# Kernel tuning notes

Measured on AMD Instinct MI355X. Metric: run time of the kernel, lower is better.

## Reference

```python
import jax, jax.numpy as jnp
import numpy as np

NTYPES = 2
MAXNEI = 100
MNT = MAXNEI * NTYPES  # max_neighbor * ntypes = 200
RMIN = 0.5
RMAX = 6.0
M1 = 100   # last embedding width
M2 = 16
FH = 240   # fitting hidden width
NPHYS = 4
TFEAT = 8
B, NAT = 4, 1024


def mlp_resnet(x, Ws, bs):
    # DeepMD-style MLP: tanh layers with identity / duplicated-identity resnet
    for W, b in zip(Ws, bs):
        h = jnp.tanh(x @ W + b)
        if h.shape[-1] == x.shape[-1]:
            h = h + x
        elif h.shape[-1] == 2 * x.shape[-1]:
            h = h + jnp.concatenate([x, x], axis=-1)
        x = h
    return x


def setup_inputs() -> dict:
    key = jax.random.key(0)
    ks = jax.random.split(key, 24)
    r = jax.random.uniform(ks[0], (B, NAT, MNT), minval=0.1, maxval=7.0)
    pad = jax.random.uniform(ks[1], (B, NAT, MNT)) < 0.25
    r = jnp.where(pad, 0.0, r)
    d = jax.random.normal(ks[2], (B, NAT, MNT, 3))
    d = d / jnp.linalg.norm(d, axis=-1, keepdims=True)
    ImageDR = jnp.concatenate([r[..., None], r[..., None] * d], axis=-1).astype(jnp.float32)

    list_neigh = jax.random.randint(ks[3], (B, NAT, MNT), 0, MAXNEI)
    Imagetype_map = jax.random.randint(ks[4], (NAT,), 0, NTYPES).astype(jnp.int32)
    type_map = jnp.array([3, 14], dtype=jnp.int64)

    davg = (0.1 * jax.random.normal(ks[5], (NTYPES, MNT, 4))).astype(jnp.float32)
    dstd = (1.0 + 0.1 * jax.random.uniform(ks[6], (NTYPES, MNT, 4))).astype(jnp.float32)

    def w(k, shape):
        return (jax.random.normal(k, shape) / np.sqrt(shape[-2] if len(shape) > 1 else 1.0)).astype(jnp.float32)

    type_vector = jax.random.normal(ks[7], (NTYPES, NPHYS)).astype(jnp.float32)
    tW0 = w(ks[8], (NPHYS, TFEAT)); tb0 = jnp.zeros((TFEAT,), jnp.float32)
    eW0 = w(ks[9], (1 + TFEAT, 25)); eb0 = jnp.zeros((25,), jnp.float32)
    eW1 = w(ks[10], (25, 50));       eb1 = jnp.zeros((50,), jnp.float32)
    eW2 = w(ks[11], (50, M1));       eb2 = jnp.zeros((M1,), jnp.float32)
    fW0 = w(ks[12], (NTYPES, M2 * M1, FH)); fb0 = jnp.zeros((NTYPES, FH), jnp.float32)
    fW1 = w(ks[13], (NTYPES, FH, FH));      fb1 = jnp.zeros((NTYPES, FH), jnp.float32)
    fW2 = w(ks[14], (NTYPES, FH, FH));      fb2 = jnp.zeros((NTYPES, FH), jnp.float32)
    fWf = w(ks[15], (NTYPES, FH, 1))
    energy_shift = jnp.array([-3.2, -5.1], jnp.float32).reshape(NTYPES, 1)
    fbf = (0.01 * jax.random.normal(ks[16], (NTYPES, 1))).astype(jnp.float32) + energy_shift

    return dict(list_neigh=list_neigh, Imagetype_map=Imagetype_map, type_map=type_map,
                ImageDR=ImageDR, nghost=0, davg=davg, dstd=dstd, type_vector=type_vector,
                tW0=tW0, tb0=tb0, eW0=eW0, eb0=eb0, eW1=eW1, eb1=eb1, eW2=eW2, eb2=eb2,
                fW0=fW0, fb0=fb0, fW1=fW1, fb1=fb1, fW2=fW2, fb2=fb2, fWf=fWf, fbf=fbf)


def _forward(ImageDR, davg, dstd, type_vector, tW0, tb0, eW0, eb0, eW1, eb1, eW2, eb2,
             fW0, fb0, fW1, fb1, fW2, fb2, fWf, fbf, Imagetype_map):
    r = ImageDR[..., 0]
    r_safe = jnp.where(r > 1e-5, r, 1.0)
    inv_r = 1.0 / r_safe
    u = (r - RMIN) / (RMAX - RMIN)
    s_mid = inv_r * (u ** 3 * (-6.0 * u ** 2 + 15.0 * u - 10.0) + 1.0)
    Srij = jnp.where((r > 0) & (r < RMIN), inv_r,
                     jnp.where((r >= RMIN) & (r < RMAX), s_mid, 0.0))  # (B,N,J)
    mask = (jnp.abs(r) > 1e-5)[..., None]
    Ri = jnp.concatenate([Srij[..., None],
                          jnp.where(mask, Srij[..., None] * ImageDR[..., 1:4] * inv_r[..., None], 0.0)],
                         axis=-1)  # (B,N,J,4)
    # per-atom-type normalization
    Ri = (Ri - davg[Imagetype_map][None]) / dstd[Imagetype_map][None]

    # neighbor type feature from type-embedding net
    nt_idx = jnp.arange(MNT) // MAXNEI              # (J,) neighbor slot -> type
    tfeat = mlp_resnet(type_vector, [tW0], [tb0])   # (ntypes, TFEAT)
    nf = jnp.broadcast_to(tfeat[nt_idx][None, None], Ri.shape[:3] + (TFEAT,))
    x = jnp.concatenate([Ri[..., 0:1], nf], axis=-1)            # (B,N,J,1+TFEAT)
    G = mlp_resnet(x, [eW0, eW1, eW2], [eb0, eb1, eb2])         # (B,N,J,M1)

    xyz = jnp.einsum('bnjd,bnjm->bndm', Ri, G) / MNT            # (B,N,4,M1)
    DR = jnp.einsum('bndm,bndq->bnmq', xyz, xyz[..., :M2])      # (B,N,M1,M2)
    DR = DR.reshape(DR.shape[0], DR.shape[1], M1 * M2)

    Ei = jnp.zeros(DR.shape[:2], DR.dtype)
    for t in range(NTYPES):  # per-type fitting nets
        h = mlp_resnet(DR, [fW0[t], fW1[t], fW2[t]], [fb0[t], fb1[t], fb2[t]])
        e = (h @ fWf[t] + fbf[t])[..., 0]
        Ei = jnp.where(Imagetype_map[None, :] == t, e, Ei)
    Etot = jnp.sum(Ei, axis=1, keepdims=True)  # (B,1)
    return Etot, Ei


def reference(list_neigh, Imagetype_map, type_map, ImageDR, nghost, davg, dstd, type_vector,
              tW0, tb0, eW0, eb0, eW1, eb1, eW2, eb2,
              fW0, fb0, fW1, fb1, fW2, fb2, fWf, fbf):
    # list_neigh/type_map/nghost only participate in force computation (is_calc_f=False path)
    return _forward(ImageDR, davg, dstd, type_vector, tW0, tb0, eW0, eb0, eW1, eb1, eW2, eb2,
                    fW0, fb0, fW1, fb1, fW2, fb2, fWf, fbf, Imagetype_map)
```

## Files before the change

kernel.cpp:

```cpp
#include <hip/hip_runtime.h>
#include <hip/hip_bf16.h>

#define NATC  1024
#define BATCH 4
#define MNTC  200
#define M1C   100
#define M2C   16
#define FHC   240
#define KPAD  256
#define HSTR  264
#define H1STR 40
#define H2STR 72
#define NR    128

typedef __attribute__((ext_vector_type(8))) short bf16x8;
typedef __attribute__((ext_vector_type(4))) float f32x4;

__device__ __forceinline__ float fast_tanh(float x){
    float e = __expf(2.0f * x);
    float r = __fdividef(1.0f, e + 1.0f);
    return fmaf(-2.0f, r, 1.0f);
}

__device__ __forceinline__ unsigned short f2bf(float x){
    __hip_bfloat16 h = __float2bfloat16(x);
    return *reinterpret_cast<unsigned short*>(&h);
}

__device__ __forceinline__ float bf2f(unsigned short u){
    unsigned int v = ((unsigned int)u) << 16;
    return *reinterpret_cast<float*>(&v);
}

__device__ __forceinline__ unsigned int pack2(float a, float b){
    return (unsigned int)f2bf(a) | ((unsigned int)f2bf(b) << 16);
}

__global__ __launch_bounds__(256) void part_kernel(const int* __restrict__ tmap,
                                                   int* __restrict__ idx,
                                                   int* __restrict__ counts){
    __shared__ int s0[256], s1[256];
    const int tid = threadIdx.x;
    int ty[4]; int c0 = 0, c1 = 0;
    #pragma unroll
    for (int r = 0; r < 4; ++r){
        ty[r] = tmap[tid*4 + r];
        if (ty[r] == 0) c0++; else c1++;
    }
    s0[tid] = c0; s1[tid] = c1;
    __syncthreads();
    for (int off = 1; off < 256; off <<= 1){
        int v0 = (tid >= off) ? s0[tid-off] : 0;
        int v1 = (tid >= off) ? s1[tid-off] : 0;
        __syncthreads();
        s0[tid] += v0; s1[tid] += v1;
        __syncthreads();
    }
    int e0 = s0[tid] - c0, e1 = s1[tid] - c1;
    #pragma unroll
    for (int r = 0; r < 4; ++r){
        int n = tid*4 + r;
        if (ty[r] == 0) idx[e0++] = n; else idx[NATC + e1++] = n;
    }
    if (tid == 255){ counts[0] = s0[255]; counts[1] = s1[255]; }
}

__global__ __launch_bounds__(256) void transp_kernel(const float* __restrict__ src,
                                                     unsigned short* __restrict__ dst,
                                                     int K, int N, int Kpad, int nkt, int nnt){
    __shared__ float tile[64][65];
    const int tid = threadIdx.x;
    int bid = blockIdx.x;
    const int t  = bid / (nkt*nnt);
    bid -= t*nkt*nnt;
    const int kt = bid / nnt;
    const int nt = bid - kt*nnt;
    const float* s = src + (size_t)t*K*N;
    unsigned short* d = dst + (size_t)t*N*Kpad;

    const int c  = tid & 63;
    const int rg = tid >> 6;
    #pragma unroll
    for (int p = 0; p < 16; ++p){
        int row = p*4 + rg;
        int gr = kt*64 + row, gc = nt*64 + c;
        tile[row][c] = (gr < K && gc < N) ? s[(size_t)gr*N + gc] : 0.0f;
    }
    __syncthreads();
    const int nn0 = tid >> 3;
    const int k8  = (tid & 7) * 8;
    #pragma unroll
    for (int p = 0; p < 2; ++p){
        int nn = p*32 + nn0;
        int gn = nt*64 + nn;
        int gk = kt*64 + k8;
        if (gn < N && gk < Kpad){
            unsigned short v[8];
            #pragma unroll
            for (int j = 0; j < 8; ++j) v[j] = f2bf(tile[k8+j][nn]);
            *(bf16x8*)(d + (size_t)gn*Kpad + gk) = *(bf16x8*)v;
        }
    }
}

__global__ __launch_bounds__(256) void prep_kernel(const float* __restrict__ tv,
                                                   const float* __restrict__ tW0,
                                                   const float* __restrict__ tb0,
                                                   const float* __restrict__ eW0,
                                                   const float* __restrict__ eb0,
                                                   const float* __restrict__ eW1,
                                                   const float* __restrict__ eW2,
                                                   unsigned short* __restrict__ ew1t,
                                                   unsigned short* __restrict__ ew2t,
                                                   float* __restrict__ Tb){
    __shared__ float tfl[16];
    const int tid = threadIdx.x;
    if (tid < 16){
        int t = tid >> 3, f = tid & 7;
        float s = tb0[f];
        #pragma unroll
        for (int p = 0; p < 4; ++p) s = fmaf(tv[t*4+p], tW0[p*8+f], s);
        tfl[tid] = fast_tanh(s) + tv[t*4 + (f & 3)];
    }
    __syncthreads();
    if (tid < 64){
        int t = tid >> 5, o = tid & 31;
        if (o < 25){
            float s = eb0[o];
            #pragma unroll
            for (int k = 0; k < 8; ++k) s = fmaf(tfl[t*8 + k], eW0[(k+1)*25 + o], s);
            Tb[t*32 + o] = s;
        } else {
            Tb[t*32 + o] = 0.0f;
        }
    }
    for (int i = tid; i < 112*64; i += 256){
        int n = i >> 6, k = i & 63;
        ew2t[i] = (n < M1C && k < 50) ? f2bf(eW2[(size_t)k*M1C + n]) : (unsigned short)0;
    }
    for (int i = tid; i < 64*32; i += 256){
        int n = i >> 5, k = i & 31;
        ew1t[i] = (n < 50 && k < 25) ? f2bf(eW1[(size_t)k*50 + n]) : (unsigned short)0;
    }
}

__global__ __launch_bounds__(256, 4) void embed_kernel(
    const float4* __restrict__ imdr,
    const float4* __restrict__ davg,
    const float4* __restrict__ dstd,
    const int*    __restrict__ tmap,
    const float*  __restrict__ eW0,
    const float*  __restrict__ Tb,
    const float*  __restrict__ eb1,
    const float*  __restrict__ eb2,
    const unsigned short* __restrict__ ew1t,
    const unsigned short* __restrict__ ew2t,
    float* __restrict__ xyzg)
{
    __shared__ __align__(16) float Rif[NR][4];
    __shared__ __align__(16) unsigned short H1s[NR][H1STR];
    __shared__ __align__(16) unsigned short H2s[NR][H2STR];

    const int tid = threadIdx.x;
    const int bid = blockIdx.x;
    const int a   = bid >> 1;
    const int jh  = bid & 1;
    const int n0  = a & (NATC - 1);
    const int itype = tmap[n0];

    if (tid < NR){
        const int jg = jh*NR + tid;
        unsigned int* rowp = (unsigned int*)&H1s[tid][0];
        if (jg < MNTC){
            float4 dr = imdr[(size_t)a*MNTC + jg];
            float r  = dr.x;
            float rs = (r > 1e-5f) ? r : 1.0f;
            float ir = __fdividef(1.0f, rs);
            float u  = (r - 0.5f) * (1.0f/5.5f);
            float u2 = u*u, u3 = u2*u;
            float smid = ir * (u3 * (-6.0f*u2 + 15.0f*u - 10.0f) + 1.0f);
            float S = 0.0f;
            if (r > 0.0f && r < 0.5f)       S = ir;
            else if (r >= 0.5f && r < 6.0f) S = smid;
            bool msk = fabsf(r) > 1e-5f;
            float R0 = S;
            float R1 = msk ? S * dr.y * ir : 0.0f;
            float R2 = msk ? S * dr.z * ir : 0.0f;
            float R3 = msk ? S * dr.w * ir : 0.0f;
            float4 av = davg[itype*MNTC + jg];
            float4 sv = dstd[itype*MNTC + jg];
            float rin0 = __fdividef(R0 - av.x, sv.x);
            float rin1 = __fdividef(R1 - av.y, sv.y);
            float rin2 = __fdividef(R2 - av.z, sv.z);
            float rin3 = __fdividef(R3 - av.w, sv.w);
            Rif[tid][0] = rin0; Rif[tid][1] = rin1; Rif[tid][2] = rin2; Rif[tid][3] = rin3;

            const float* tb = Tb + ((jg >= 100) ? 32 : 0);
            float h1[25];
            #pragma unroll
            for (int o = 0; o < 25; ++o)
                h1[o] = fast_tanh(fmaf(rin0, eW0[o], tb[o]));

            #pragma unroll
            for (int c = 0; c < 12; ++c) rowp[c] = pack2(h1[2*c], h1[2*c+1]);
            rowp[12] = (unsigned int)f2bf(h1[24]);
            #pragma unroll
            for (int c = 13; c < 20; ++c) rowp[c] = 0u;
        } else {
            Rif[tid][0] = 0.0f; Rif[tid][1] = 0.0f; Rif[tid][2] = 0.0f; Rif[tid][3] = 0.0f;
            #pragma unroll
            for (int c = 0; c < 20; ++c) rowp[c] = 0u;
        }
    }
    __syncthreads();

    const int lane = tid & 63;
    const int w    = tid >> 6;
    const int lc   = lane & 15;
    const int lg   = lane >> 4;

    #pragma unroll
    for (int mi = 0; mi < 2; ++mi){
        const int mt = w + mi*4;
        bf16x8 af = *(const bf16x8*)&H1s[mt*16 + lc][lg*8];
        const int rbase = mt*16 + lg*4;
        #pragma unroll
        for (int nt = 0; nt < 4; ++nt){
            const int n = nt*16 + lc;
            const bool live = (n < 50);
            float bv = live ? eb1[n] : 0.0f;
            f32x4 c;
            c[0] = bv; c[1] = bv; c[2] = bv; c[3] = bv;
            bf16x8 bfr = *(const bf16x8*)(ew1t + n*32 + lg*8);
            c = __builtin_amdgcn_mfma_f32_16x16x32_bf16(af, bfr, c, 0, 0, 0);
            const int rc = n % 25;
            #pragma unroll
            for (int i = 0; i < 4; ++i){
                const int row = rbase + i;
                unsigned short v = 0;
                if (live) v = f2bf(fast_tanh(c[i]) + bf2f(H1s[row][rc]));
                H2s[row][n] = v;
            }
        }
    }
    __syncthreads();

    float* xyzp = (float*)&H1s[0][0];

    #pragma unroll
    for (int half = 0; half < 2; ++half){
        const int ntbase = half * 4;
        float xacc[4][4];
        #pragma unroll
        for (int q = 0; q < 4; ++q)
            #pragma unroll
            for (int d = 0; d < 4; ++d) xacc[q][d] = 0.0f;

        #pragma unroll
        for (int mi = 0; mi < 2; ++mi){
            const int mt = w + mi*4;
            const int rbase = mt*16 + lg*4;
            float4 rj[4];
            #pragma unroll
            for (int i = 0; i < 4; ++i) rj[i] = *(const float4*)&Rif[rbase + i][0];
            const unsigned short* arow = &H2s[mt*16 + lc][0];
            bf16x8 a0 = *(const bf16x8*)(arow + lg*8);
            bf16x8 a1 = *(const bf16x8*)(arow + 32 + lg*8);
            #pragma unroll
            for (int q = 0; q < 4; ++q){
                const int nt = ntbase + q;
                if (nt >= 7) continue;
                const int cg = nt*16 + lc;
                const unsigned short* bp = ew2t + (size_t)cg*64 + lg*8;
                bf16x8 b0 = *(const bf16x8*)(bp);
                bf16x8 b1 = *(const bf16x8*)(bp + 32);
                float bv = (cg < M1C) ? eb2[cg] : 0.0f;
                f32x4 c;
                c[0] = bv; c[1] = bv; c[2] = bv; c[3] = bv;
                c = __builtin_amdgcn_mfma_f32_16x16x32_bf16(a0, b0, c, 0, 0, 0);
                c = __builtin_amdgcn_mfma_f32_16x16x32_bf16(a1, b1, c, 0, 0, 0);
                const int rc = (cg >= 100) ? cg - 100 : ((cg >= 50) ? cg - 50 : cg);
                #pragma unroll
                for (int i = 0; i < 4; ++i){
                    float g = fast_tanh(c[i]) + bf2f(H2s[rbase + i][rc]);
                    xacc[q][0] = fmaf(g, rj[i].x, xacc[q][0]);
                    xacc[q][1] = fmaf(g, rj[i].y, xacc[q][1]);
                    xacc[q][2] = fmaf(g, rj[i].z, xacc[q][2]);
                    xacc[q][3] = fmaf(g, rj[i].w, xacc[q][3]);
                }
            }
        }
        #pragma unroll
        for (int q = 0; q < 4; ++q){
            const int nt = ntbase + q;
            if (nt >= 7) continue;
            #pragma unroll
            for (int d = 0; d < 4; ++d){
                float v = xacc[q][d];
                v += __shfl_xor(v, 16);
                v += __shfl_xor(v, 32);
                if (lane < 16) xyzp[((w*4 + d)*112) + nt*16 + lc] = v;
            }
        }
    }
    __syncthreads();

    for (int i = tid; i < 448; i += 256){
        int d = i / 112, m = i - d*112;
        xyzg[(size_t)a*896 + jh*448 + i] =
            xyzp[(0*4+d)*112 + m] + xyzp[(1*4+d)*112 + m] +
            xyzp[(2*4+d)*112 + m] + xyzp[(3*4+d)*112 + m];
    }
}

__global__ __launch_bounds__(256) void dr_kernel(const float* __restrict__ xyzg,
                                                 unsigned short* __restrict__ DRout){
    __shared__ float xyzs[448];
    const int a = blockIdx.x;
    const int tid = threadIdx.x;
    for (int i = tid; i < 448; i += 256)
        xyzs[i] = (xyzg[(size_t)a*896 + i] + xyzg[(size_t)a*896 + 448 + i]) * (1.0f / (float)MNTC);
    __syncthreads();
    if (tid < 200){
        const int i8 = tid * 8;
        const int m  = i8 >> 4;
        const int qb = i8 & 15;
        float xm[4], s[8];
        #pragma unroll
        for (int d = 0; d < 4; ++d) xm[d] = xyzs[d*112 + m];
        #pragma unroll
        for (int e = 0; e < 8; ++e){
            float acc = 0.0f;
            #pragma unroll
            for (int d = 0; d < 4; ++d) acc = fmaf(xm[d], xyzs[d*112 + qb + e], acc);
            s[e] = acc;
        }
        unsigned short v[8];
        #pragma unroll
        for (int e = 0; e < 8; ++e) v[e] = f2bf(s[e]);
        *(bf16x8*)(DRout + (size_t)a*(M1C*M2C) + i8) = *(bf16x8*)v;
    }
}

__global__ __launch_bounds__(512, 2) void fitm_kernel(
    const unsigned short* __restrict__ DRbf,
    const int*   __restrict__ idx,
    const int*   __restrict__ counts,
    const unsigned short* __restrict__ w0t,
    const unsigned short* __restrict__ w1t,
    const unsigned short* __restrict__ w2t,
    const float* __restrict__ fb0,
    const float* __restrict__ fb1,
    const float* __restrict__ fb2,
    const float* __restrict__ fWf,
    const float* __restrict__ fbf,
    float* __restrict__ out)
{
    const int bid = blockIdx.x;
    const int t = bid & 1;
    const int g = (bid >> 1) & 31;
    const int b = bid >> 6;
    const int cnt  = counts[t];
    const int base = g * 32;
    if (base >= cnt) return;
    const int na = min(32, cnt - base);

    __shared__ int ns[32];
    __shared__ __align__(16) unsigned short hA[32][HSTR];
    __shared__ __align__(16) unsigned short hB[32][HSTR];
    __shared__ float epart[8][32];

    const int tid  = threadIdx.x;
    const int lane = tid & 63;
    const int w    = tid >> 6;
    if (tid < 32) ns[tid] = idx[t*NATC + base + ((tid < na) ? tid : 0)];
    __syncthreads();

    const int lc = lane & 15;
    const int lg = lane >> 4;

    int   ncol[2];  bool act[2];
    #pragma unroll
    for (int nt = 0; nt < 2; ++nt){
        ncol[nt] = w*32 + nt*16 + lc;
        act[nt]  = (w*32 + nt*16) < FHC;
    }

    const unsigned short* aptr[2];
    aptr[0] = DRbf + ((size_t)(b*NATC + ns[lc]))*1600 + lg*8;
    aptr[1] = DRbf + ((size_t)(b*NATC + ns[16 + lc]))*1600 + lg*8;
    const unsigned short* bptr0[2];
    #pragma unroll
    for (int nt = 0; nt < 2; ++nt)
        bptr0[nt] = act[nt] ? (w0t + ((size_t)(t*FHC + ncol[nt]))*1600 + lg*8) : w0t;

    f32x4 acc[2][2];
    #pragma unroll
    for (int mi = 0; mi < 2; ++mi)
        #pragma unroll
        for (int nt = 0; nt < 2; ++nt){
            float bv = act[nt] ? fb0[t*FHC + ncol[nt]] : 0.0f;
            acc[mi][nt][0] = bv; acc[mi][nt][1] = bv; acc[mi][nt][2] = bv; acc[mi][nt][3] = bv;
        }
    #pragma unroll 4
    for (int ks = 0; ks < 50; ++ks){
        bf16x8 a0 = *(const bf16x8*)(aptr[0] + ks*32);
        bf16x8 a1 = *(const bf16x8*)(aptr[1] + ks*32);
        #pragma unroll
        for (int nt = 0; nt < 2; ++nt){
            if (act[nt]){
                bf16x8 bfg = *(const bf16x8*)(bptr0[nt] + ks*32);
                acc[0][nt] = __builtin_amdgcn_mfma_f32_16x16x32_bf16(a0, bfg, acc[0][nt], 0, 0, 0);
                acc[1][nt] = __builtin_amdgcn_mfma_f32_16x16x32_bf16(a1, bfg, acc[1][nt], 0, 0, 0);
            }
        }
    }
    float h0r[2][2][4];
    #pragma unroll
    for (int mi = 0; mi < 2; ++mi)
        #pragma unroll
        for (int nt = 0; nt < 2; ++nt)
            #pragma unroll
            for (int i = 0; i < 4; ++i){
                int row = mi*16 + lg*4 + i;
                if (act[nt]){
                    h0r[mi][nt][i] = fast_tanh(acc[mi][nt][i]);
                    hA[row][ncol[nt]] = f2bf(h0r[mi][nt][i]);
                } else {
                    h0r[mi][nt][i] = 0.0f;
                    hA[row][ncol[nt]] = 0;
                }
            }
    __syncthreads();

    f32x4 acc1[2][2];
    #pragma unroll
    for (int mi = 0; mi < 2; ++mi)
        #pragma unroll
        for (int nt = 0; nt < 2; ++nt){
            float bv = act[nt] ? fb1[t*FHC + ncol[nt]] : 0.0f;
            acc1[mi][nt][0] = bv; acc1[mi][nt][1] = bv; acc1[mi][nt][2] = bv; acc1[mi][nt][3] = bv;
        }
    const unsigned short* b1p[2];
    #pragma unroll
    for (int nt = 0; nt < 2; ++nt)
        b1p[nt] = act[nt] ? (w1t + ((size_t)(t*FHC + ncol[nt]))*KPAD + lg*8) : w1t;
    #pragma unroll
    for (int ks = 0; ks < 8; ++ks){
        bf16x8 a0 = *(const bf16x8*)&hA[lc][ks*32 + lg*8];
        bf16x8 a1 = *(const bf16x8*)&hA[16 + lc][ks*32 + lg*8];
        #pragma unroll
        for (int nt = 0; nt < 2; ++nt){
            if (act[nt]){
                bf16x8 bfg = *(const bf16x8*)(b1p[nt] + ks*32);
                acc1[0][nt] = __builtin_amdgcn_mfma_f32_16x16x32_bf16(a0, bfg, acc1[0][nt], 0, 0, 0);
                acc1[1][nt] = __builtin_amdgcn_mfma_f32_16x16x32_bf16(a1, bfg, acc1[1][nt], 0, 0, 0);
            }
        }
    }
    float h1r[2][2][4];
    #pragma unroll
    for (int mi = 0; mi < 2; ++mi)
        #pragma unroll
        for (int nt = 0; nt < 2; ++nt)
            #pragma unroll
            for (int i = 0; i < 4; ++i){
                int row = mi*16 + lg*4 + i;
                if (act[nt]){
                    h1r[mi][nt][i] = fast_tanh(acc1[mi][nt][i]) + h0r[mi][nt][i];
                    hB[row][ncol[nt]] = f2bf(h1r[mi][nt][i]);
                } else {
                    h1r[mi][nt][i] = 0.0f;
                    hB[row][ncol[nt]] = 0;
                }
            }
    __syncthreads();

    f32x4 acc2[2][2];
    #pragma unroll
    for (int mi = 0; mi < 2; ++mi)
        #pragma unroll
        for (int nt = 0; nt < 2; ++nt){
            float bv = act[nt] ? fb2[t*FHC + ncol[nt]] : 0.0f;
            acc2[mi][nt][0] = bv; acc2[mi][nt][1] = bv; acc2[mi][nt][2] = bv; acc2[mi][nt][3] = bv;
        }
    const unsigned short* b2p[2];
    #pragma unroll
    for (int nt = 0; nt < 2; ++nt)
        b2p[nt] = act[nt] ? (w2t + ((size_t)(t*FHC + ncol[nt]))*KPAD + lg*8) : w2t;
    #pragma unroll
    for (int ks = 0; ks < 8; ++ks){
        bf16x8 a0 = *(const bf16x8*)&hB[lc][ks*32 + lg*8];
        bf16x8 a1 = *(const bf16x8*)&hB[16 + lc][ks*32 + lg*8];
        #pragma unroll
        for (int nt = 0; nt < 2; ++nt){
            if (act[nt]){
                bf16x8 bfg = *(const bf16x8*)(b2p[nt] + ks*32);
                acc2[0][nt] = __builtin_amdgcn_mfma_f32_16x16x32_bf16(a0, bfg, acc2[0][nt], 0, 0, 0);
                acc2[1][nt] = __builtin_amdgcn_mfma_f32_16x16x32_bf16(a1, bfg, acc2[1][nt], 0, 0, 0);
            }
        }
    }

    float p[2][4];
    #pragma unroll
    for (int mi = 0; mi < 2; ++mi)
        #pragma unroll
        for (int i = 0; i < 4; ++i) p[mi][i] = 0.0f;
    #pragma unroll
    for (int nt = 0; nt < 2; ++nt){
        if (act[nt]){
            float wfv = fWf[t*FHC + ncol[nt]];
            #pragma unroll
            for (int mi = 0; mi < 2; ++mi)
                #pragma unroll
                for (int i = 0; i < 4; ++i){
                    float h = fast_tanh(acc2[mi][nt][i]) + h1r[mi][nt][i];
                    p[mi][i] = fmaf(h, wfv, p[mi][i]);
                }
        }
    }
    #pragma unroll
    for (int off = 1; off < 16; off <<= 1){
        #pragma unroll
        for (int mi = 0; mi < 2; ++mi)
            #pragma unroll
            for (int i = 0; i < 4; ++i)
                p[mi][i] += __shfl_xor(p[mi][i], off);
    }
    if (lc == 0){
        #pragma unroll
        for (int mi = 0; mi < 2; ++mi)
            #pragma unroll
            for (int i = 0; i < 4; ++i)
                epart[w][mi*16 + lg*4 + i] = p[mi][i];
    }
    __syncthreads();
    if (tid < 32){
        float e = fbf[t];
        #pragma unroll
        for (int ww = 0; ww < 8; ++ww) e += epart[ww][tid];
        float ee = 0.0f;
        if (tid < na){
            out[4 + b*NATC + ns[tid]] = e;
            ee = e;
        }
        #pragma unroll
        for (int off = 16; off >= 1; off >>= 1) ee += __shfl_down(ee, off, 32);
        if (tid == 0) atomicAdd(&out[b], ee);
    }
}

extern "C" void kernel_launch(void* const* d_in, const int* in_sizes, int n_in,
                              void* d_out, int out_size, void* d_ws, size_t ws_size,
                              hipStream_t stream)
{
    (void)in_sizes; (void)n_in; (void)out_size; (void)ws_size;
    const int*   tmap = (const int*)d_in[1];
    const float* imdr = (const float*)d_in[3];
    const float* davg = (const float*)d_in[5];
    const float* dstd = (const float*)d_in[6];
    const float* tv   = (const float*)d_in[7];
    const float* tW0  = (const float*)d_in[8];
    const float* tb0  = (const float*)d_in[9];
    const float* eW0  = (const float*)d_in[10];
    const float* eb0  = (const float*)d_in[11];
    const float* eW1  = (const float*)d_in[12];
    const float* eb1  = (const float*)d_in[13];
    const float* eW2  = (const float*)d_in[14];
    const float* eb2  = (const float*)d_in[15];
    const float* fW0  = (const float*)d_in[16];
    const float* fb0  = (const float*)d_in[17];
    const float* fW1  = (const float*)d_in[18];
    const float* fb1  = (const float*)d_in[19];
    const float* fW2  = (const float*)d_in[20];
    const float* fb2  = (const float*)d_in[21];
    const float* fWf  = (const float*)d_in[22];
    const float* fbf  = (const float*)d_in[23];
    float* out = (float*)d_out;

    char* ws = (char*)d_ws;
    int*   counts = (int*)ws;
    int*   idx    = (int*)(ws + 64);
    unsigned short* DRbf = (unsigned short*)(ws + 16384);
    unsigned short* w0t  = DRbf + (size_t)BATCH*NATC*1600;
    unsigned short* w1t  = w0t + (size_t)2*FHC*1600;
    unsigned short* w2t  = w1t + (size_t)2*FHC*KPAD;
    unsigned short* ew2t = w2t + (size_t)2*FHC*KPAD;
    unsigned short* ew1t = ew2t + 112*64;
    float* Tb            = (float*)(ew1t + 64*32);
    float* xyzg          = (float*)((char*)Tb + 4096);

    hipMemsetAsync(d_out, 0, 4*sizeof(float), stream);
    part_kernel<<<1, 256, 0, stream>>>(tmap, idx, counts);
    prep_kernel<<<1, 256, 0, stream>>>(tv, tW0, tb0, eW0, eb0, eW1, eW2, ew1t, ew2t, Tb);
    transp_kernel<<<2*25*4, 256, 0, stream>>>(fW0, w0t, 1600, FHC, 1600, 25, 4);
    transp_kernel<<<2*4*4,  256, 0, stream>>>(fW1, w1t, FHC, FHC, KPAD, 4, 4);
    transp_kernel<<<2*4*4,  256, 0, stream>>>(fW2, w2t, FHC, FHC, KPAD, 4, 4);
    embed_kernel<<<2*BATCH*NATC, 256, 0, stream>>>(
        (const float4*)imdr, (const float4*)davg, (const float4*)dstd, tmap,
        eW0, Tb, eb1, eb2, ew1t, ew2t, xyzg);
    dr_kernel<<<BATCH*NATC, 256, 0, stream>>>(xyzg, DRbf);
    fitm_kernel<<<256, 512, 0, stream>>>(
        DRbf, idx, counts, w0t, w1t, w2t, fb0, fb1, fb2, fWf, fbf, out);
}
```

Baseline: 373.2 us.

## Split fused fitting net into per-layer LDS-tiled GEMM kernels

Replaces the single fused three-layer fitting kernel with separate kernels. One handles layer 0 and another, launched twice, handles layers 1 and 2; each uses 64x64 LDS-staged tiles shared by four waves. Intermediate activations go through global bf16 buffers, and the final dot product is accumulated with atomics into a per-atom buffer that a small finish kernel scatters and sums. Weights are padded to 256 output rows so tiles need no bounds checks. The aim is better operand reuse and more parallel blocks, at the cost of extra launches, global round-trips for activations, and atomics.

```diff
diff --git a/kernel.cpp b/kernel.cpp
--- a/kernel.cpp
+++ b/kernel.cpp
@@ -7,11 +7,11 @@
 #define M1C   100
 #define M2C   16
 #define FHC   240
-#define KPAD  256
-#define HSTR  264
+#define NPAD  256
 #define H1STR 40
 #define H2STR 72
 #define NR    128
+#define ASTR  72
 
 typedef __attribute__((ext_vector_type(8))) short bf16x8;
 typedef __attribute__((ext_vector_type(4))) float f32x4;
@@ -67,7 +67,8 @@
 
 __global__ __launch_bounds__(256) void transp_kernel(const float* __restrict__ src,
                                                      unsigned short* __restrict__ dst,
-                                                     int K, int N, int Kpad, int nkt, int nnt){
+                                                     int K, int N, int Npad, int Kpad,
+                                                     int nkt, int nnt){
     __shared__ float tile[64][65];
     const int tid = threadIdx.x;
     int bid = blockIdx.x;
@@ -76,7 +77,7 @@
     const int kt = bid / nnt;
     const int nt = bid - kt*nnt;
     const float* s = src + (size_t)t*K*N;
-    unsigned short* d = dst + (size_t)t*N*Kpad;
+    unsigned short* d = dst + (size_t)t*Npad*Kpad;
 
     const int c  = tid & 63;
     const int rg = tid >> 6;
@@ -94,7 +95,7 @@
         int nn = p*32 + nn0;
         int gn = nt*64 + nn;
         int gk = kt*64 + k8;
-        if (gn < N && gk < Kpad){
+        if (gn < Npad && gk < Kpad){
             unsigned short v[8];
             #pragma unroll
             for (int j = 0; j < 8; ++j) v[j] = f2bf(tile[k8+j][nn]);
@@ -342,213 +343,204 @@
     }
 }
 
-__global__ __launch_bounds__(512, 2) void fitm_kernel(
+__global__ __launch_bounds__(256, 4) void fit_l0(
     const unsigned short* __restrict__ DRbf,
     const int*   __restrict__ idx,
     const int*   __restrict__ counts,
-    const unsigned short* __restrict__ w0t,
-    const unsigned short* __restrict__ w1t,
-    const unsigned short* __restrict__ w2t,
+    const unsigned short* __restrict__ w0p,
     const float* __restrict__ fb0,
-    const float* __restrict__ fb1,
-    const float* __restrict__ fb2,
-    const float* __restrict__ fWf,
-    const float* __restrict__ fbf,
-    float* __restrict__ out)
+    unsigned short* __restrict__ h0)
 {
-    const int bid = blockIdx.x;
+    int bid = blockIdx.x;
+    const int ntile = bid & 3; bid >>= 2;
+    const int mt = bid & 15;  bid >>= 4;
     const int t = bid & 1;
-    const int g = (bid >> 1) & 31;
-    const int b = bid >> 6;
-    const int cnt  = counts[t];
-    const int base = g * 32;
-    if (base >= cnt) return;
-    const int na = min(32, cnt - base);
-
-    __shared__ int ns[32];
-    __shared__ __align__(16) unsigned short hA[32][HSTR];
-    __shared__ __align__(16) unsigned short hB[32][HSTR];
-    __shared__ float epart[8][32];
-
-    const int tid  = threadIdx.x;
-    const int lane = tid & 63;
-    const int w    = tid >> 6;
-    if (tid < 32) ns[tid] = idx[t*NATC + base + ((tid < na) ? tid : 0)];
-    __syncthreads();
-
-    const int lc = lane & 15;
-    const int lg = lane >> 4;
-
-    int   ncol[2];  bool act[2];
-    #pragma unroll
-    for (int nt = 0; nt < 2; ++nt){
-        ncol[nt] = w*32 + nt*16 + lc;
-        act[nt]  = (w*32 + nt*16) < FHC;
-    }
-
-    const unsigned short* aptr[2];
-    aptr[0] = DRbf + ((size_t)(b*NATC + ns[lc]))*1600 + lg*8;
-    aptr[1] = DRbf + ((size_t)(b*NATC + ns[16 + lc]))*1600 + lg*8;
-    const unsigned short* bptr0[2];
-    #pragma unroll
-    for (int nt = 0; nt < 2; ++nt)
-        bptr0[nt] = act[nt] ? (w0t + ((size_t)(t*FHC + ncol[nt]))*1600 + lg*8) : w0t;
+    const int b = bid >> 1;
+    const int cnt = counts[t];
+    const int mbase = mt*64;
+    if (mbase >= cnt) return;
+
+    __shared__ int ns[64];
+    __shared__ __align__(16) unsigned short As[64][ASTR];
+    __shared__ __align__(16) unsigned short Bs[64][ASTR];
+
+    const int tid = threadIdx.x;
+    if (tid < 64) ns[tid] = idx[t*NATC + min(mbase + tid, cnt - 1)];
+    __syncthreads();
+
+    const int lane = tid & 63, w = tid >> 6;
+    const int wm = w >> 1, wn = w & 1;
+    const int lc = lane & 15, lg = lane >> 4;
+
+    const int srow = tid >> 3;
+    const int scol = (tid & 7) * 8;
+
+    const unsigned short* arow0 = DRbf + ((size_t)(b*NATC + ns[srow]))*1600;
+    const unsigned short* arow1 = DRbf + ((size_t)(b*NATC + ns[srow + 32]))*1600;
+    const unsigned short* brow0 = w0p + ((size_t)(t*NPAD + ntile*64 + srow))*1600;
+    const unsigned short* brow1 = w0p + ((size_t)(t*NPAD + ntile*64 + srow + 32))*1600;
 
     f32x4 acc[2][2];
     #pragma unroll
     for (int mi = 0; mi < 2; ++mi)
         #pragma unroll
-        for (int nt = 0; nt < 2; ++nt){
-            float bv = act[nt] ? fb0[t*FHC + ncol[nt]] : 0.0f;
-            acc[mi][nt][0] = bv; acc[mi][nt][1] = bv; acc[mi][nt][2] = bv; acc[mi][nt][3] = bv;
-        }
-    #pragma unroll 4
-    for (int ks = 0; ks < 50; ++ks){
-        bf16x8 a0 = *(const bf16x8*)(aptr[0] + ks*32);
-        bf16x8 a1 = *(const bf16x8*)(aptr[1] + ks*32);
-        #pragma unroll
-        for (int nt = 0; nt < 2; ++nt){
-            if (act[nt]){
-                bf16x8 bfg = *(const bf16x8*)(bptr0[nt] + ks*32);
-                acc[0][nt] = __builtin_amdgcn_mfma_f32_16x16x32_bf16(a0, bfg, acc[0][nt], 0, 0, 0);
-                acc[1][nt] = __builtin_amdgcn_mfma_f32_16x16x32_bf16(a1, bfg, acc[1][nt], 0, 0, 0);
+        for (int ni = 0; ni < 2; ++ni){
+            int col = ntile*64 + wn*32 + ni*16 + lc;
+            float bv = (col < FHC) ? fb0[t*FHC + col] : 0.0f;
+            acc[mi][ni][0] = bv; acc[mi][ni][1] = bv;
+            acc[mi][ni][2] = bv; acc[mi][ni][3] = bv;
+        }
+
+    for (int kc = 0; kc < 1600; kc += 64){
+        __syncthreads();
+        *(bf16x8*)&As[srow][scol]      = *(const bf16x8*)(arow0 + kc + scol);
+        *(bf16x8*)&As[srow + 32][scol] = *(const bf16x8*)(arow1 + kc + scol);
+        *(bf16x8*)&Bs[srow][scol]      = *(const bf16x8*)(brow0 + kc + scol);
+        *(bf16x8*)&Bs[srow + 32][scol] = *(const bf16x8*)(brow1 + kc + scol);
+        __syncthreads();
+        #pragma unroll
+        for (int kk = 0; kk < 2; ++kk){
+            bf16x8 a0 = *(const bf16x8*)&As[wm*32 + lc][kk*32 + lg*8];
+            bf16x8 a1 = *(const bf16x8*)&As[wm*32 + 16 + lc][kk*32 + lg*8];
+            bf16x8 b0 = *(const bf16x8*)&Bs[wn*32 + lc][kk*32 + lg*8];
+            bf16x8 b1 = *(const bf16x8*)&Bs[wn*32 + 16 + lc][kk*32 + lg*8];
+            acc[0][0] = __builtin_amdgcn_mfma_f32_16x16x32_bf16(a0, b0, acc[0][0], 0, 0, 0);
+            acc[0][1] = __builtin_amdgcn_mfma_f32_16x16x32_bf16(a0, b1, acc[0][1], 0, 0, 0);
+            acc[1][0] = __builtin_amdgcn_mfma_f32_16x16x32_bf16(a1, b0, acc[1][0], 0, 0, 0);
+            acc[1][1] = __builtin_amdgcn_mfma_f32_16x16x32_bf16(a1, b1, acc[1][1], 0, 0, 0);
+        }
+    }
+
+    const size_t Rseg = (size_t)((b*2 + t)*1024 + mbase);
+    #pragma unroll
+    for (int mi = 0; mi < 2; ++mi)
+        #pragma unroll
+        for (int ni = 0; ni < 2; ++ni){
+            int col = ntile*64 + wn*32 + ni*16 + lc;
+            #pragma unroll
+            for (int i = 0; i < 4; ++i){
+                int rowl = wm*32 + mi*16 + lg*4 + i;
+                h0[(Rseg + rowl)*NPAD + col] = f2bf(fast_tanh(acc[mi][ni][i]));
             }
         }
-    }
-    float h0r[2][2][4];
+}
+
+__global__ __launch_bounds__(256, 4) void fit_l12(
+    const unsigned short* __restrict__ h_in,
+    const int*   __restrict__ counts,
+    const unsigned short* __restrict__ wp,
+    const float* __restrict__ fb,
+    const float* __restrict__ wf,
+    unsigned short* __restrict__ h_out,
+    float* __restrict__ Ei_buf)
+{
+    int bid = blockIdx.x;
+    const int ntile = bid & 3; bid >>= 2;
+    const int mt = bid & 15;  bid >>= 4;
+    const int t = bid & 1;
+    const int b = bid >> 1;
+    const int cnt = counts[t];
+    const int mbase = mt*64;
+    if (mbase >= cnt) return;
+
+    __shared__ __align__(16) unsigned short As[64][ASTR];
+    __shared__ __align__(16) unsigned short Bs[64][ASTR];
+
+    const int tid = threadIdx.x;
+    const int lane = tid & 63, w = tid >> 6;
+    const int wm = w >> 1, wn = w & 1;
+    const int lc = lane & 15, lg = lane >> 4;
+
+    const int srow = tid >> 3;
+    const int scol = (tid & 7) * 8;
+
+    const size_t Rseg = (size_t)((b*2 + t)*1024 + mbase);
+    const unsigned short* arow0 = h_in + (Rseg + srow)*NPAD;
+    const unsigned short* arow1 = h_in + (Rseg + srow + 32)*NPAD;
+    const unsigned short* brow0 = wp + ((size_t)(t*NPAD + ntile*64 + srow))*NPAD;
+    const unsigned short* brow1 = wp + ((size_t)(t*NPAD + ntile*64 + srow + 32))*NPAD;
+
+    f32x4 acc[2][2];
     #pragma unroll
     for (int mi = 0; mi < 2; ++mi)
         #pragma unroll
-        for (int nt = 0; nt < 2; ++nt)
+        for (int ni = 0; ni < 2; ++ni){
+            int col = ntile*64 + wn*32 + ni*16 + lc;
+            float bv = (col < FHC) ? fb[t*FHC + col] : 0.0f;
+            acc[mi][ni][0] = bv; acc[mi][ni][1] = bv;
+            acc[mi][ni][2] = bv; acc[mi][ni][3] = bv;
+        }
+
+    for (int kc = 0; kc < 256; kc += 64){
+        __syncthreads();
+        *(bf16x8*)&As[srow][scol]      = *(const bf16x8*)(arow0 + kc + scol);
+        *(bf16x8*)&As[srow + 32][scol] = *(const bf16x8*)(arow1 + kc + scol);
+        *(bf16x8*)&Bs[srow][scol]      = *(const bf16x8*)(brow0 + kc + scol);
+        *(bf16x8*)&Bs[srow + 32][scol] = *(const bf16x8*)(brow1 + kc + scol);
+        __syncthreads();
+        #pragma unroll
+        for (int kk = 0; kk < 2; ++kk){
+            bf16x8 a0 = *(const bf16x8*)&As[wm*32 + lc][kk*32 + lg*8];
+            bf16x8 a1 = *(const bf16x8*)&As[wm*32 + 16 + lc][kk*32 + lg*8];
+            bf16x8 b0 = *(const bf16x8*)&Bs[wn*32 + lc][kk*32 + lg*8];
+            bf16x8 b1 = *(const bf16x8*)&Bs[wn*32 + 16 + lc][kk*32 + lg*8];
+            acc[0][0] = __builtin_amdgcn_mfma_f32_16x16x32_bf16(a0, b0, acc[0][0], 0, 0, 0);
+            acc[0][1] = __builtin_amdgcn_mfma_f32_16x16x32_bf16(a0, b1, acc[0][1], 0, 0, 0);
+            acc[1][0] = __builtin_amdgcn_mfma_f32_16x16x32_bf16(a1, b0, acc[1][0], 0, 0, 0);
+            acc[1][1] = __builtin_amdgcn_mfma_f32_16x16x32_bf16(a1, b1, acc[1][1], 0, 0, 0);
+        }
+    }
+
+    const bool fuse = (wf != nullptr);
+    #pragma unroll
+    for (int mi = 0; mi < 2; ++mi){
+        float pr[4] = {0.0f, 0.0f, 0.0f, 0.0f};
+        #pragma unroll
+        for (int ni = 0; ni < 2; ++ni){
+            int col = ntile*64 + wn*32 + ni*16 + lc;
+            float wfv = 0.0f;
+            if (fuse) wfv = (col < FHC) ? wf[t*FHC + col] : 0.0f;
             #pragma unroll
             for (int i = 0; i < 4; ++i){
-                int row = mi*16 + lg*4 + i;
-                if (act[nt]){
-                    h0r[mi][nt][i] = fast_tanh(acc[mi][nt][i]);
-                    hA[row][ncol[nt]] = f2bf(h0r[mi][nt][i]);
-                } else {
-                    h0r[mi][nt][i] = 0.0f;
-                    hA[row][ncol[nt]] = 0;
+                int rowl = wm*32 + mi*16 + lg*4 + i;
+                size_t gaddr = (Rseg + rowl)*NPAD + col;
+                float hv = fast_tanh(acc[mi][ni][i]) + bf2f(h_in[gaddr]);
+                if (!fuse) h_out[gaddr] = f2bf(hv);
+                else       pr[i] = fmaf(hv, wfv, pr[i]);
+            }
+        }
+        if (fuse){
+            #pragma unroll
+            for (int i = 0; i < 4; ++i){
+                float v = pr[i];
+                v += __shfl_xor(v, 1); v += __shfl_xor(v, 2);
+                v += __shfl_xor(v, 4); v += __shfl_xor(v, 8);
+                if (lc == 0){
+                    int rowl = wm*32 + mi*16 + lg*4 + i;
+                    atomicAdd(&Ei_buf[Rseg + rowl], v);
                 }
             }
-    __syncthreads();
-
-    f32x4 acc1[2][2];
-    #pragma unroll
-    for (int mi = 0; mi < 2; ++mi)
-        #pragma unroll
-        for (int nt = 0; nt < 2; ++nt){
-            float bv = act[nt] ? fb1[t*FHC + ncol[nt]] : 0.0f;
-            acc1[mi][nt][0] = bv; acc1[mi][nt][1] = bv; acc1[mi][nt][2] = bv; acc1[mi][nt][3] = bv;
-        }
-    const unsigned short* b1p[2];
-    #pragma unroll
-    for (int nt = 0; nt < 2; ++nt)
-        b1p[nt] = act[nt] ? (w1t + ((size_t)(t*FHC + ncol[nt]))*KPAD + lg*8) : w1t;
-    #pragma unroll
-    for (int ks = 0; ks < 8; ++ks){
-        bf16x8 a0 = *(const bf16x8*)&hA[lc][ks*32 + lg*8];
-        bf16x8 a1 = *(const bf16x8*)&hA[16 + lc][ks*32 + lg*8];
-        #pragma unroll
-        for (int nt = 0; nt < 2; ++nt){
-            if (act[nt]){
-                bf16x8 bfg = *(const bf16x8*)(b1p[nt] + ks*32);
-                acc1[0][nt] = __builtin_amdgcn_mfma_f32_16x16x32_bf16(a0, bfg, acc1[0][nt], 0, 0, 0);
-                acc1[1][nt] = __builtin_amdgcn_mfma_f32_16x16x32_bf16(a1, bfg, acc1[1][nt], 0, 0, 0);
-            }
-        }
-    }
-    float h1r[2][2][4];
-    #pragma unroll
-    for (int mi = 0; mi < 2; ++mi)
-        #pragma unroll
-        for (int nt = 0; nt < 2; ++nt)
-            #pragma unroll
-            for (int i = 0; i < 4; ++i){
-                int row = mi*16 + lg*4 + i;
-                if (act[nt]){
-                    h1r[mi][nt][i] = fast_tanh(acc1[mi][nt][i]) + h0r[mi][nt][i];
-                    hB[row][ncol[nt]] = f2bf(h1r[mi][nt][i]);
-                } else {
-                    h1r[mi][nt][i] = 0.0f;
-                    hB[row][ncol[nt]] = 0;
-                }
-            }
-    __syncthreads();
-
-    f32x4 acc2[2][2];
-    #pragma unroll
-    for (int mi = 0; mi < 2; ++mi)
-        #pragma unroll
-        for (int nt = 0; nt < 2; ++nt){
-            float bv = act[nt] ? fb2[t*FHC + ncol[nt]] : 0.0f;
-            acc2[mi][nt][0] = bv; acc2[mi][nt][1] = bv; acc2[mi][nt][2] = bv; acc2[mi][nt][3] = bv;
-        }
-    const unsigned short* b2p[2];
-    #pragma unroll
-    for (int nt = 0; nt < 2; ++nt)
-        b2p[nt] = act[nt] ? (w2t + ((size_t)(t*FHC + ncol[nt]))*KPAD + lg*8) : w2t;
-    #pragma unroll
-    for (int ks = 0; ks < 8; ++ks){
-        bf16x8 a0 = *(const bf16x8*)&hB[lc][ks*32 + lg*8];
-        bf16x8 a1 = *(const bf16x8*)&hB[16 + lc][ks*32 + lg*8];
-        #pragma unroll
-        for (int nt = 0; nt < 2; ++nt){
-            if (act[nt]){
-                bf16x8 bfg = *(const bf16x8*)(b2p[nt] + ks*32);
-                acc2[0][nt] = __builtin_amdgcn_mfma_f32_16x16x32_bf16(a0, bfg, acc2[0][nt], 0, 0, 0);
-                acc2[1][nt] = __builtin_amdgcn_mfma_f32_16x16x32_bf16(a1, bfg, acc2[1][nt], 0, 0, 0);
-            }
-        }
-    }
-
-    float p[2][4];
-    #pragma unroll
-    for (int mi = 0; mi < 2; ++mi)
-        #pragma unroll
-        for (int i = 0; i < 4; ++i) p[mi][i] = 0.0f;
-    #pragma unroll
-    for (int nt = 0; nt < 2; ++nt){
-        if (act[nt]){
-            float wfv = fWf[t*FHC + ncol[nt]];
-            #pragma unroll
-            for (int mi = 0; mi < 2; ++mi)
-                #pragma unroll
-                for (int i = 0; i < 4; ++i){
-                    float h = fast_tanh(acc2[mi][nt][i]) + h1r[mi][nt][i];
-                    p[mi][i] = fmaf(h, wfv, p[mi][i]);
-                }
-        }
-    }
-    #pragma unroll
-    for (int off = 1; off < 16; off <<= 1){
-        #pragma unroll
-        for (int mi = 0; mi < 2; ++mi)
-            #pragma unroll
-            for (int i = 0; i < 4; ++i)
-                p[mi][i] += __shfl_xor(p[mi][i], off);
-    }
-    if (lc == 0){
-        #pragma unroll
-        for (int mi = 0; mi < 2; ++mi)
-            #pragma unroll
-            for (int i = 0; i < 4; ++i)
-                epart[w][mi*16 + lg*4 + i] = p[mi][i];
-    }
-    __syncthreads();
-    if (tid < 32){
-        float e = fbf[t];
-        #pragma unroll
-        for (int ww = 0; ww < 8; ++ww) e += epart[ww][tid];
-        float ee = 0.0f;
-        if (tid < na){
-            out[4 + b*NATC + ns[tid]] = e;
-            ee = e;
-        }
-        #pragma unroll
-        for (int off = 16; off >= 1; off >>= 1) ee += __shfl_down(ee, off, 32);
-        if (tid == 0) atomicAdd(&out[b], ee);
-    }
+        }
+    }
+}
+
+__global__ __launch_bounds__(256) void finish_kernel(const float* __restrict__ Ei_buf,
+                                                     const int* __restrict__ idx,
+                                                     const int* __restrict__ counts,
+                                                     const float* __restrict__ fbf,
+                                                     float* __restrict__ out){
+    const int gid = blockIdx.x*256 + threadIdx.x;
+    const int b = gid >> 11;
+    const int t = (gid >> 10) & 1;
+    const int k = gid & 1023;
+    float e = 0.0f;
+    if (k < counts[t]){
+        e = Ei_buf[gid] + fbf[t];
+        out[4 + b*NATC + idx[t*NATC + k]] = e;
+    }
+    #pragma unroll
+    for (int off = 1; off < 64; off <<= 1) e += __shfl_xor(e, off);
+    if ((threadIdx.x & 63) == 0) atomicAdd(&out[b], e);
 }
 
 extern "C" void kernel_launch(void* const* d_in, const int* in_sizes, int n_in,
@@ -583,24 +575,30 @@
     int*   counts = (int*)ws;
     int*   idx    = (int*)(ws + 64);
     unsigned short* DRbf = (unsigned short*)(ws + 16384);
-    unsigned short* w0t  = DRbf + (size_t)BATCH*NATC*1600;
-    unsigned short* w1t  = w0t + (size_t)2*FHC*1600;
-    unsigned short* w2t  = w1t + (size_t)2*FHC*KPAD;
-    unsigned short* ew2t = w2t + (size_t)2*FHC*KPAD;
+    unsigned short* w0p  = DRbf + (size_t)BATCH*NATC*1600;
+    unsigned short* w1p  = w0p + (size_t)2*NPAD*1600;
+    unsigned short* w2p  = w1p + (size_t)2*NPAD*NPAD;
+    unsigned short* ew2t = w2p + (size_t)2*NPAD*NPAD;
     unsigned short* ew1t = ew2t + 112*64;
     float* Tb            = (float*)(ew1t + 64*32);
     float* xyzg          = (float*)((char*)Tb + 4096);
+    unsigned short* h0   = (unsigned short*)(xyzg + (size_t)BATCH*NATC*896);
+    unsigned short* h1   = h0 + (size_t)8192*NPAD;
+    float* Ei_buf        = (float*)(h1 + (size_t)8192*NPAD);
 
     hipMemsetAsync(d_out, 0, 4*sizeof(float), stream);
+    hipMemsetAsync(Ei_buf, 0, 8192*sizeof(float), stream);
     part_kernel<<<1, 256, 0, stream>>>(tmap, idx, counts);
     prep_kernel<<<1, 256, 0, stream>>>(tv, tW0, tb0, eW0, eb0, eW1, eW2, ew1t, ew2t, Tb);
-    transp_kernel<<<2*25*4, 256, 0, stream>>>(fW0, w0t, 1600, FHC, 1600, 25, 4);
-    transp_kernel<<<2*4*4,  256, 0, stream>>>(fW1, w1t, FHC, FHC, KPAD, 4, 4);
-    transp_kernel<<<2*4*4,  256, 0, stream>>>(fW2, w2t, FHC, FHC, KPAD, 4, 4);
+    transp_kernel<<<2*25*4, 256, 0, stream>>>(fW0, w0p, 1600, FHC, NPAD, 1600, 25, 4);
+    transp_kernel<<<2*4*4,  256, 0, stream>>>(fW1, w1p, FHC, FHC, NPAD, NPAD, 4, 4);
+    transp_kernel<<<2*4*4,  256, 0, stream>>>(fW2, w2p, FHC, FHC, NPAD, NPAD, 4, 4);
     embed_kernel<<<2*BATCH*NATC, 256, 0, stream>>>(
         (const float4*)imdr, (const float4*)davg, (const float4*)dstd, tmap,
         eW0, Tb, eb1, eb2, ew1t, ew2t, xyzg);
     dr_kernel<<<BATCH*NATC, 256, 0, stream>>>(xyzg, DRbf);
-    fitm_kernel<<<256, 512, 0, stream>>>(
-        DRbf, idx, counts, w0t, w1t, w2t, fb0, fb1, fb2, fWf, fbf, out);
-}
+    fit_l0<<<BATCH*2*16*4, 256, 0, stream>>>(DRbf, idx, counts, w0p, fb0, h0);
+    fit_l12<<<BATCH*2*16*4, 256, 0, stream>>>(h0, counts, w1p, fb1, nullptr, h1, Ei_buf);
+    fit_l12<<<BATCH*2*16*4, 256, 0, stream>>>(h1, counts, w2p, fb2, fWf, h0, Ei_buf);
+    finish_kernel<<<32, 256, 0, stream>>>(Ei_buf, idx, counts, fbf, out);
+}
```

New measurement: 357.1 us. -4.3%, faster.
